# Performance work log

Measured on AMD Instinct MI355X. Metric: run time of the kernel, lower is better.

Reference implementation:

```python
import jax, jax.numpy as jnp
import numpy as np

MAX_AREA_WIDTH = 3  # from init_kwargs


def _window_vals(val, width, merge):
    """Multi-scale forward window sums: for each w in 1..width, sum val[t:t+w]
    over the seq axis, concatenated along the seq axis (total length
    width*L - width*(width-1)/2). Equivalent to the torch recurrence."""
    B, H, L, D = val.shape
    csum = jnp.concatenate(
        [jnp.zeros((B, H, 1, D), val.dtype), jnp.cumsum(val, axis=2)], axis=2)
    parts = []
    for i in range(width):
        w = i + 1
        s = csum[:, :, w:, :] - csum[:, :, :L - w + 1, :]  # [B,H,L-i,D]
        if merge == 'mean':
            s = s / jnp.asarray(w, val.dtype)
        parts.append(s)
    return jnp.concatenate(parts, axis=2)


def _window_masks(mask, width, zero_pad):
    parts = [mask[:, :, :, i:] for i in range(width)]
    m = jnp.concatenate(parts, axis=-1)  # [B,H,L,L']
    if zero_pad:
        m = m.at[:, :, 0, :].set(0)
    return m


def setup_inputs() -> dict:
    key = jax.random.key(0)
    kq, kk, kv = jax.random.split(key, 3)
    B, H, L, D = 8, 8, 512, 64
    q = jax.random.normal(kq, (B, H, L, D), jnp.float32)
    k = jax.random.normal(kk, (B, H, L, D), jnp.float32)
    v = jax.random.normal(kv, (B, H, L, D), jnp.float32)
    # causal attention mask, as used in pykt knowledge-tracing models
    mask = jnp.broadcast_to(jnp.tril(jnp.ones((L, L), jnp.int32)), (B, H, L, L))
    return {"q": q, "k": k, "v": v, "d_k": 64, "mask": mask, "zero_pad": 1}


def reference(q, k, v, d_k, mask, zero_pad):
    W = MAX_AREA_WIDTH
    k_area = _window_vals(k, W, 'mean')   # [B,H,L',D]
    v_area = _window_vals(v, W, 'sum')    # [B,H,L',D]
    m = _window_masks(mask, W, zero_pad)  # [B,H,L,L']
    scores = jnp.einsum('bhqd,bhkd->bhqk', q, k_area) / jnp.sqrt(
        jnp.asarray(d_k, jnp.float32))
    scores = jnp.where(m == 0, jnp.asarray(-1e32, scores.dtype), scores)
    attn = jax.nn.softmax(scores, axis=-1)  # dropout omitted (eval / p=0)
    return jnp.einsum('bhqk,bhkd->bhqd', attn, v_area)
```

## Files before the change

kernel.cpp:

```cpp
#include <hip/hip_runtime.h>


#define LSEQ 512
#define DDIM 64
#define BQ 64
#define BK 64
#define NTH 256

typedef __attribute__((ext_vector_type(8))) short bf8_t;
typedef __attribute__((ext_vector_type(4))) float f32x4;

__device__ __forceinline__ unsigned short f2bf(float f) {
  union { float f; unsigned u; } v; v.f = f;
  unsigned u = v.u;
  unsigned r = u + 0x7fffu + ((u >> 16) & 1u);
  return (unsigned short)(r >> 16);
}
__device__ __forceinline__ float bf2f(unsigned short h) {
  union { unsigned u; float f; } v; v.u = ((unsigned)h) << 16; return v.f;
}
__device__ __forceinline__ unsigned pk2(float a, float b) {
  return (unsigned)f2bf(a) | ((unsigned)f2bf(b) << 16);
}
__device__ __forceinline__ float ex2(float x) {
  float r; asm("v_exp_f32 %0, %1" : "=v"(r) : "v"(x)); return r;
}
__device__ __forceinline__ bf8_t pack8(float4 a, float4 b, float s) {
  bf8_t r;
  r[0] = (short)f2bf(a.x * s); r[1] = (short)f2bf(a.y * s);
  r[2] = (short)f2bf(a.z * s); r[3] = (short)f2bf(a.w * s);
  r[4] = (short)f2bf(b.x * s); r[5] = (short)f2bf(b.y * s);
  r[6] = (short)f2bf(b.z * s); r[7] = (short)f2bf(b.w * s);
  return r;
}

__global__ __launch_bounds__(256)
void vt_kernel(const float* __restrict__ vg, unsigned short* __restrict__ vt) {
  const int bh = blockIdx.x >> 3, oct = blockIdx.x & 7;
  const float* vb = vg + (size_t)bh * LSEQ * DDIM;
  unsigned short* vo = vt + (size_t)bh * DDIM * LSEQ;
#pragma unroll
  for (int it = 0; it < 4; ++it) {
    int item = threadIdx.x + it * 256;
    int d = item & 63, tq = item >> 6;
    int t = oct * 64 + tq * 4;
    ushort4 o;
    o.x = f2bf(vb[(t + 0) * DDIM + d]);
    o.y = f2bf(vb[(t + 1) * DDIM + d]);
    o.z = f2bf(vb[(t + 2) * DDIM + d]);
    o.w = f2bf(vb[(t + 3) * DDIM + d]);
    *(ushort4*)&vo[(size_t)d * LSEQ + t] = o;
  }
}

__global__ __launch_bounds__(256, 3)
void area_attn_kernel(const float* __restrict__ qg,
                      const float* __restrict__ kg,
                      const unsigned short* __restrict__ vtg,
                      float* __restrict__ outg) {
  const int bid = blockIdx.x;
  const int tid = threadIdx.x;

  __shared__ __align__(16) unsigned short Kbf[64 * 72];
  __shared__ __align__(16) unsigned short Vt[64 * 72];
  __shared__ __align__(16) unsigned short Ps[64 * 72];
  __shared__ __align__(16) float Ss[64][68];
  __shared__ float scale_arr[64];
  __shared__ float l_arr[64];

  if (bid >= 512) {
    const int bh = bid - 512;
    const unsigned short* vb = vtg + (size_t)bh * DDIM * LSEQ;
    float4* red = (float4*)&Ss[0][0];
    const int d4 = tid & 15, rg = tid >> 4;
    float4 acc = make_float4(0.f, 0.f, 0.f, 0.f);
    for (int t = rg; t < LSEQ; t += 16) {
      float c = (t == 0 || t == LSEQ - 1) ? 3.f
              : (t == 1 || t == LSEQ - 2) ? 5.f : 6.f;
      int d0 = d4 * 4;
      acc.x += c * bf2f(vb[(size_t)(d0 + 0) * LSEQ + t]);
      acc.y += c * bf2f(vb[(size_t)(d0 + 1) * LSEQ + t]);
      acc.z += c * bf2f(vb[(size_t)(d0 + 2) * LSEQ + t]);
      acc.w += c * bf2f(vb[(size_t)(d0 + 3) * LSEQ + t]);
    }
    red[rg * 16 + d4] = acc;
    __syncthreads();
    if (rg == 0) {
      float4 s = make_float4(0.f, 0.f, 0.f, 0.f);
#pragma unroll
      for (int g = 0; g < 16; ++g) {
        float4 x = red[g * 16 + d4];
        s.x += x.x; s.y += x.y; s.z += x.z; s.w += x.w;
      }
      const float inv = 1.0f / 1533.0f;
      s.x *= inv; s.y *= inv; s.z *= inv; s.w *= inv;
      ((float4*)(outg + (size_t)bh * LSEQ * DDIM))[d4] = s;
    }
    return;
  }

  const int half = bid >> 8;
  const int qt = half ? (7 - (bid & 7)) : (bid & 7);
  const int bh = ((bid >> 3) & 31) + (half << 5);
  const int q0 = qt * BQ;

  const float* qb = qg + (size_t)bh * LSEQ * DDIM;
  const float* kb = kg + (size_t)bh * LSEQ * DDIM;
  const unsigned short* vtb = vtg + (size_t)bh * DDIM * LSEQ;

  const int lane = tid & 63, w = tid >> 6;
  const int lc = lane & 15, lg = lane >> 4;
  const int koff = lg * 8;
  const int pr = tid >> 2, ps = tid & 3;
  const int ec0 = ps * 16;
  const float L2E = 1.44269504088896341f;

  bf8_t qa0, qa1;
  {
    const float* qrp = qb + (size_t)(q0 + 16 * w + lc) * DDIM;
    float4 xa = *(const float4*)(qrp + koff);
    float4 xb = *(const float4*)(qrp + koff + 4);
    qa0 = pack8(xa, xb, 0.125f);
    xa = *(const float4*)(qrp + 32 + koff);
    xb = *(const float4*)(qrp + 36 + koff);
    qa1 = pack8(xa, xb, 0.125f);
  }

  f32x4 oacc[4];
#pragma unroll
  for (int nt = 0; nt < 4; ++nt) oacc[nt] = (f32x4){0.f, 0.f, 0.f, 0.f};
  float m_run = -3.0e38f, l_run = 0.f;

  const int ntiles = qt + 1;
  for (int kt = 0; kt < ntiles; ++kt) {
    const int t0 = kt * BK;

    if (ps == 0) {
      if (kt == 0) { Ss[pr][64] = -1.0e30f; Ss[pr][65] = -1.0e30f; }
      else         { Ss[pr][64] = Ss[pr][62]; Ss[pr][65] = Ss[pr][63]; }
    }
    __syncthreads();

    {
      const float4* ka = (const float4*)(kb + (size_t)t0 * DDIM);
#pragma unroll
      for (int it = 0; it < 4; ++it) {
        int f = tid + it * NTH;
        int t = f >> 4, c4 = f & 15;
        float4 x = ka[t * 16 + c4];
        ushort4 o;
        o.x = f2bf(x.x); o.y = f2bf(x.y); o.z = f2bf(x.z); o.w = f2bf(x.w);
        *(ushort4*)&Kbf[t * 72 + c4 * 4] = o;
      }
#pragma unroll
      for (int it = 0; it < 4; ++it) {
        int f = tid + it * NTH;
        int d = f >> 4, tq = f & 15;
        ushort4 x = *(const ushort4*)&vtb[(size_t)d * LSEQ + t0 + tq * 4];
        *(ushort4*)&Vt[d * 72 + tq * 4] = x;
      }
      if (tid < 64) {
        unsigned x = 0;
        if (kt > 0) x = *(const unsigned*)&vtb[(size_t)tid * LSEQ + t0 - 2];
        *(unsigned*)&Vt[tid * 72 + 64] = x;
      }
    }
    __syncthreads();

#pragma unroll
    for (int nt = 0; nt < 4; ++nt) {
      int key = nt * 16 + lc;
      bf8_t kb0 = *(const bf8_t*)&Kbf[key * 72 + koff];
      bf8_t kb1 = *(const bf8_t*)&Kbf[key * 72 + 32 + koff];
      f32x4 acc = (f32x4){0.f, 0.f, 0.f, 0.f};
      acc = __builtin_amdgcn_mfma_f32_16x16x32_bf16(qa0, kb0, acc, 0, 0, 0);
      acc = __builtin_amdgcn_mfma_f32_16x16x32_bf16(qa1, kb1, acc, 0, 0, 0);
#pragma unroll
      for (int r = 0; r < 4; ++r)
        Ss[16 * w + 4 * lg + r][nt * 16 + lc] = acc[r];
    }

    {
      const int vmax = q0 + pr - t0;
      float pm1, pm2;
      if (ps == 0) { pm1 = Ss[pr][65] * L2E; pm2 = Ss[pr][64] * L2E; }
      else         { pm1 = Ss[pr][ec0 - 1] * L2E; pm2 = Ss[pr][ec0 - 2] * L2E; }

      float sv[16];
      *(float4*)&sv[0]  = *(const float4*)&Ss[pr][ec0];
      *(float4*)&sv[4]  = *(const float4*)&Ss[pr][ec0 + 4];
      *(float4*)&sv[8]  = *(const float4*)&Ss[pr][ec0 + 8];
      *(float4*)&sv[12] = *(const float4*)&Ss[pr][ec0 + 12];
#pragma unroll
      for (int k = 0; k < 16; ++k) sv[k] *= L2E;

      float mloc = -3.0e38f;
      {
        float a1 = pm1, a2 = pm2;
#pragma unroll
        for (int k = 0; k < 16; ++k) {
          float s0 = sv[k];
          float t = a1 + s0;
          float mm = fmaxf(s0, fmaxf(0.5f * t, (1.0f / 3.0f) * (a2 + t)));
          if (ec0 + k <= vmax) mloc = fmaxf(mloc, mm);
          a2 = a1; a1 = s0;
        }
      }
      mloc = fmaxf(mloc, __shfl_xor(mloc, 1));
      mloc = fmaxf(mloc, __shfl_xor(mloc, 2));
      const float m_new = fmaxf(m_run, mloc);
      const float alpha = ex2(m_run - m_new);
      m_run = m_new;
      if (ps == 0) scale_arr[pr] = alpha;
      l_run *= alpha;

      float cf[18];
#pragma unroll
      for (int k = 0; k < 18; ++k) cf[k] = 0.f;
      float ladd = 0.f;
      {
        float a1 = pm1, a2 = pm2;
#pragma unroll
        for (int k = 0; k < 16; ++k) {
          float s0 = sv[k];
          bool vld = (ec0 + k) <= vmax;
          float t = a1 + s0;
          float p1 = vld ? ex2(s0 - m_new) : 0.f;
          float p2 = vld ? ex2(0.5f * t - m_new) : 0.f;
          float p3 = vld ? ex2((1.0f / 3.0f) * (a2 + t) - m_new) : 0.f;
          float p23 = p2 + p3, p123 = p1 + p23;
          ladd += p123;
          cf[k + 2] += p123;
          cf[k + 1] += p23;
          cf[k]     += p3;
          a2 = a1; a1 = s0;
        }
      }
      ladd += __shfl_xor(ladd, 1);
      ladd += __shfl_xor(ladd, 2);
      l_run += ladd;
      if (ps == 0) l_arr[pr] = l_run;

      float up16 = __shfl_up(cf[16], 1, 4);
      float up17 = __shfl_up(cf[17], 1, 4);
      if (ps > 0) { cf[0] += up16; cf[1] += up17; }

      const int base = pr * 72;
      if (ps == 0) {
        *(unsigned*)&Ps[base + 64] = pk2(cf[0], cf[1]);
#pragma unroll
        for (int j = 0; j < 7; ++j)
          *(unsigned*)&Ps[base + 2 * j] = pk2(cf[2 + 2 * j], cf[3 + 2 * j]);
      } else {
        const int tcb = 16 * ps - 2;
#pragma unroll
        for (int j = 0; j < 8; ++j)
          *(unsigned*)&Ps[base + tcb + 2 * j] = pk2(cf[2 * j], cf[2 * j + 1]);
        if (ps == 3) *(unsigned*)&Ps[base + 62] = pk2(cf[16], cf[17]);
      }
    }

    {
      float al[4];
#pragma unroll
      for (int r = 0; r < 4; ++r) al[r] = scale_arr[16 * w + 4 * lg + r];
#pragma unroll
      for (int nt = 0; nt < 4; ++nt)
#pragma unroll
        for (int r = 0; r < 4; ++r) oacc[nt][r] *= al[r];

      bf8_t pa0 = *(const bf8_t*)&Ps[(16 * w + lc) * 72 + koff];
      bf8_t pa1 = *(const bf8_t*)&Ps[(16 * w + lc) * 72 + 32 + koff];
      float cm2[4], cm1[4];
#pragma unroll
      for (int r = 0; r < 4; ++r) {
        unsigned pc = *(const unsigned*)&Ps[(16 * w + 4 * lg + r) * 72 + 64];
        cm2[r] = bf2f((unsigned short)(pc & 0xffffu));
        cm1[r] = bf2f((unsigned short)(pc >> 16));
      }
#pragma unroll
      for (int nt = 0; nt < 4; ++nt) {
        int d = nt * 16 + lc;
        bf8_t vb0 = *(const bf8_t*)&Vt[d * 72 + koff];
        bf8_t vb1 = *(const bf8_t*)&Vt[d * 72 + 32 + koff];
        oacc[nt] = __builtin_amdgcn_mfma_f32_16x16x32_bf16(pa0, vb0, oacc[nt], 0, 0, 0);
        oacc[nt] = __builtin_amdgcn_mfma_f32_16x16x32_bf16(pa1, vb1, oacc[nt], 0, 0, 0);
        unsigned vc = *(const unsigned*)&Vt[d * 72 + 64];
        float vm2 = bf2f((unsigned short)(vc & 0xffffu));
        float vm1 = bf2f((unsigned short)(vc >> 16));
#pragma unroll
        for (int r = 0; r < 4; ++r)
          oacc[nt][r] += cm2[r] * vm2 + cm1[r] * vm1;
      }
    }
  }

  {
#pragma unroll
    for (int r = 0; r < 4; ++r) {
      int row = 16 * w + 4 * lg + r;
      int gr = q0 + row;
      if (gr != 0) {
        float inv = 1.0f / l_arr[row];
#pragma unroll
        for (int nt = 0; nt < 4; ++nt)
          outg[(size_t)(bh * LSEQ + gr) * DDIM + nt * 16 + lc] = oacc[nt][r] * inv;
      }
    }
  }
}

extern "C" void kernel_launch(void* const* d_in, const int* in_sizes, int n_in,
                              void* d_out, int out_size, void* d_ws, size_t ws_size,
                              hipStream_t stream) {
  (void)in_sizes; (void)n_in; (void)ws_size; (void)out_size;
  const float* q = (const float*)d_in[0];
  const float* k = (const float*)d_in[1];
  const float* v = (const float*)d_in[2];
  float* out = (float*)d_out;
  unsigned short* vt = (unsigned short*)d_ws;

  vt_kernel<<<dim3(512), dim3(256), 0, stream>>>(v, vt);
  area_attn_kernel<<<dim3(512 + 64), dim3(256), 0, stream>>>(q, k, vt, out);
}
```

Before: 146.3 us.

## Prefetch next K/V tile into registers and widen LDS row stride

```diff
diff --git a/kernel.cpp b/kernel.cpp
--- a/kernel.cpp
+++ b/kernel.cpp
@@ -6,6 +6,7 @@
 #define BQ 64
 #define BK 64
 #define NTH 256
+#define SPB 88
 
 typedef __attribute__((ext_vector_type(8))) short bf8_t;
 typedef __attribute__((ext_vector_type(4))) float f32x4;
@@ -61,9 +62,9 @@
   const int bid = blockIdx.x;
   const int tid = threadIdx.x;
 
-  __shared__ __align__(16) unsigned short Kbf[64 * 72];
-  __shared__ __align__(16) unsigned short Vt[64 * 72];
-  __shared__ __align__(16) unsigned short Ps[64 * 72];
+  __shared__ __align__(16) unsigned short Kbf[64 * SPB];
+  __shared__ __align__(16) unsigned short Vt[64 * SPB];
+  __shared__ __align__(16) unsigned short Ps[64 * SPB];
   __shared__ __align__(16) float Ss[64][68];
   __shared__ float scale_arr[64];
   __shared__ float l_arr[64];
@@ -126,12 +127,32 @@
     qa1 = pack8(xa, xb, 0.125f);
   }
 
+  float4 kpre[4];
+  ushort4 vpre[4];
+  unsigned cpre = 0;
+  auto issue_pf = [&](int t0p) {
+    const float4* ka = (const float4*)(kb + (size_t)t0p * DDIM);
+#pragma unroll
+    for (int it = 0; it < 4; ++it) kpre[it] = ka[tid + it * NTH];
+#pragma unroll
+    for (int it = 0; it < 4; ++it) {
+      int f = tid + it * NTH;
+      int d = f >> 4, tq = f & 15;
+      vpre[it] = *(const ushort4*)&vtb[(size_t)d * LSEQ + t0p + tq * 4];
+    }
+    cpre = 0;
+    if (tid < 64 && t0p > 0)
+      cpre = *(const unsigned*)&vtb[(size_t)tid * LSEQ + t0p - 2];
+  };
+
   f32x4 oacc[4];
 #pragma unroll
   for (int nt = 0; nt < 4; ++nt) oacc[nt] = (f32x4){0.f, 0.f, 0.f, 0.f};
   float m_run = -3.0e38f, l_run = 0.f;
 
   const int ntiles = qt + 1;
+  issue_pf(0);
+
   for (int kt = 0; kt < ntiles; ++kt) {
     const int t0 = kt * BK;
 
@@ -142,36 +163,32 @@
     __syncthreads();
 
     {
-      const float4* ka = (const float4*)(kb + (size_t)t0 * DDIM);
 #pragma unroll
       for (int it = 0; it < 4; ++it) {
         int f = tid + it * NTH;
         int t = f >> 4, c4 = f & 15;
-        float4 x = ka[t * 16 + c4];
+        float4 x = kpre[it];
         ushort4 o;
         o.x = f2bf(x.x); o.y = f2bf(x.y); o.z = f2bf(x.z); o.w = f2bf(x.w);
-        *(ushort4*)&Kbf[t * 72 + c4 * 4] = o;
+        *(ushort4*)&Kbf[t * SPB + c4 * 4] = o;
       }
 #pragma unroll
       for (int it = 0; it < 4; ++it) {
         int f = tid + it * NTH;
         int d = f >> 4, tq = f & 15;
-        ushort4 x = *(const ushort4*)&vtb[(size_t)d * LSEQ + t0 + tq * 4];
-        *(ushort4*)&Vt[d * 72 + tq * 4] = x;
-      }
-      if (tid < 64) {
-        unsigned x = 0;
-        if (kt > 0) x = *(const unsigned*)&vtb[(size_t)tid * LSEQ + t0 - 2];
-        *(unsigned*)&Vt[tid * 72 + 64] = x;
-      }
+        *(ushort4*)&Vt[d * SPB + tq * 4] = vpre[it];
+      }
+      if (tid < 64) *(unsigned*)&Vt[tid * SPB + 64] = cpre;
     }
     __syncthreads();
+
+    if (kt + 1 < ntiles) issue_pf(t0 + BK);
 
 #pragma unroll
     for (int nt = 0; nt < 4; ++nt) {
       int key = nt * 16 + lc;
-      bf8_t kb0 = *(const bf8_t*)&Kbf[key * 72 + koff];
-      bf8_t kb1 = *(const bf8_t*)&Kbf[key * 72 + 32 + koff];
+      bf8_t kb0 = *(const bf8_t*)&Kbf[key * SPB + koff];
+      bf8_t kb1 = *(const bf8_t*)&Kbf[key * SPB + 32 + koff];
       f32x4 acc = (f32x4){0.f, 0.f, 0.f, 0.f};
       acc = __builtin_amdgcn_mfma_f32_16x16x32_bf16(qa0, kb0, acc, 0, 0, 0);
       acc = __builtin_amdgcn_mfma_f32_16x16x32_bf16(qa1, kb1, acc, 0, 0, 0);
@@ -245,7 +262,7 @@
       float up17 = __shfl_up(cf[17], 1, 4);
       if (ps > 0) { cf[0] += up16; cf[1] += up17; }
 
-      const int base = pr * 72;
+      const int base = pr * SPB;
       if (ps == 0) {
         *(unsigned*)&Ps[base + 64] = pk2(cf[0], cf[1]);
 #pragma unroll
@@ -269,23 +286,23 @@
 #pragma unroll
         for (int r = 0; r < 4; ++r) oacc[nt][r] *= al[r];
 
-      bf8_t pa0 = *(const bf8_t*)&Ps[(16 * w + lc) * 72 + koff];
-      bf8_t pa1 = *(const bf8_t*)&Ps[(16 * w + lc) * 72 + 32 + koff];
+      bf8_t pa0 = *(const bf8_t*)&Ps[(16 * w + lc) * SPB + koff];
+      bf8_t pa1 = *(const bf8_t*)&Ps[(16 * w + lc) * SPB + 32 + koff];
       float cm2[4], cm1[4];
 #pragma unroll
       for (int r = 0; r < 4; ++r) {
-        unsigned pc = *(const unsigned*)&Ps[(16 * w + 4 * lg + r) * 72 + 64];
+        unsigned pc = *(const unsigned*)&Ps[(16 * w + 4 * lg + r) * SPB + 64];
         cm2[r] = bf2f((unsigned short)(pc & 0xffffu));
         cm1[r] = bf2f((unsigned short)(pc >> 16));
       }
 #pragma unroll
       for (int nt = 0; nt < 4; ++nt) {
         int d = nt * 16 + lc;
-        bf8_t vb0 = *(const bf8_t*)&Vt[d * 72 + koff];
-        bf8_t vb1 = *(const bf8_t*)&Vt[d * 72 + 32 + koff];
+        bf8_t vb0 = *(const bf8_t*)&Vt[d * SPB + koff];
+        bf8_t vb1 = *(const bf8_t*)&Vt[d * SPB + 32 + koff];
         oacc[nt] = __builtin_amdgcn_mfma_f32_16x16x32_bf16(pa0, vb0, oacc[nt], 0, 0, 0);
         oacc[nt] = __builtin_amdgcn_mfma_f32_16x16x32_bf16(pa1, vb1, oacc[nt], 0, 0, 0);
-        unsigned vc = *(const unsigned*)&Vt[d * 72 + 64];
+        unsigned vc = *(const unsigned*)&Vt[d * SPB + 64];
         float vm2 = bf2f((unsigned short)(vc & 0xffffu));
         float vm1 = bf2f((unsigned short)(vc >> 16));
 #pragma unroll
```

After: 156.5 us. 1.07x slower.

## Split attention into single-wave 16-row blocks reading pre-converted bf16 operands

Applied to the files above, without the earlier changes.

```diff
diff --git a/kernel.cpp b/kernel.cpp
--- a/kernel.cpp
+++ b/kernel.cpp
@@ -3,9 +3,9 @@
 
 #define LSEQ 512
 #define DDIM 64
-#define BQ 64
 #define BK 64
-#define NTH 256
+#define SPB 88
+#define SSW 68
 
 typedef __attribute__((ext_vector_type(8))) short bf8_t;
 typedef __attribute__((ext_vector_type(4))) float f32x4;
@@ -25,113 +25,106 @@
 __device__ __forceinline__ float ex2(float x) {
   float r; asm("v_exp_f32 %0, %1" : "=v"(r) : "v"(x)); return r;
 }
-__device__ __forceinline__ bf8_t pack8(float4 a, float4 b, float s) {
-  bf8_t r;
-  r[0] = (short)f2bf(a.x * s); r[1] = (short)f2bf(a.y * s);
-  r[2] = (short)f2bf(a.z * s); r[3] = (short)f2bf(a.w * s);
-  r[4] = (short)f2bf(b.x * s); r[5] = (short)f2bf(b.y * s);
-  r[6] = (short)f2bf(b.z * s); r[7] = (short)f2bf(b.w * s);
-  return r;
-}
 
 __global__ __launch_bounds__(256)
-void vt_kernel(const float* __restrict__ vg, unsigned short* __restrict__ vt) {
-  const int bh = blockIdx.x >> 3, oct = blockIdx.x & 7;
-  const float* vb = vg + (size_t)bh * LSEQ * DDIM;
-  unsigned short* vo = vt + (size_t)bh * DDIM * LSEQ;
-#pragma unroll
-  for (int it = 0; it < 4; ++it) {
-    int item = threadIdx.x + it * 256;
-    int d = item & 63, tq = item >> 6;
-    int t = oct * 64 + tq * 4;
-    ushort4 o;
-    o.x = f2bf(vb[(t + 0) * DDIM + d]);
-    o.y = f2bf(vb[(t + 1) * DDIM + d]);
-    o.z = f2bf(vb[(t + 2) * DDIM + d]);
-    o.w = f2bf(vb[(t + 3) * DDIM + d]);
-    *(ushort4*)&vo[(size_t)d * LSEQ + t] = o;
-  }
-}
-
-__global__ __launch_bounds__(256, 3)
-void area_attn_kernel(const float* __restrict__ qg,
-                      const float* __restrict__ kg,
-                      const unsigned short* __restrict__ vtg,
-                      float* __restrict__ outg) {
-  const int bid = blockIdx.x;
-  const int tid = threadIdx.x;
-
-  __shared__ __align__(16) unsigned short Kbf[64 * 72];
-  __shared__ __align__(16) unsigned short Vt[64 * 72];
-  __shared__ __align__(16) unsigned short Ps[64 * 72];
-  __shared__ __align__(16) float Ss[64][68];
-  __shared__ float scale_arr[64];
-  __shared__ float l_arr[64];
-
-  if (bid >= 512) {
-    const int bh = bid - 512;
-    const unsigned short* vb = vtg + (size_t)bh * DDIM * LSEQ;
-    float4* red = (float4*)&Ss[0][0];
+void prep_kernel(const float* __restrict__ qg, const float* __restrict__ kg,
+                 const float* __restrict__ vg,
+                 unsigned short* __restrict__ vt,
+                 unsigned short* __restrict__ qbf,
+                 unsigned short* __restrict__ kbf,
+                 float* __restrict__ outg) {
+  const int bid = blockIdx.x, tid = threadIdx.x;
+  if (bid < 512) {
+    const int bh = bid >> 3, oct = bid & 7;
+    const float* vb = vg + (size_t)bh * LSEQ * DDIM;
+    unsigned short* vo = vt + (size_t)bh * DDIM * LSEQ;
+#pragma unroll
+    for (int it = 0; it < 4; ++it) {
+      int item = tid + it * 256;
+      int d = item & 63, tq = item >> 6;
+      int t = oct * 64 + tq * 4;
+      ushort4 o;
+      o.x = f2bf(vb[(t + 0) * DDIM + d]);
+      o.y = f2bf(vb[(t + 1) * DDIM + d]);
+      o.z = f2bf(vb[(t + 2) * DDIM + d]);
+      o.w = f2bf(vb[(t + 3) * DDIM + d]);
+      *(ushort4*)&vo[(size_t)d * LSEQ + t] = o;
+    }
+  } else if (bid < 1536) {
+    const bool isq = bid < 1024;
+    const float4* src = (const float4*)(isq ? qg : kg);
+    ushort4* dst = (ushort4*)(isq ? qbf : kbf);
+    const float s = isq ? 0.125f : 1.0f;
+    const int blk = bid & 511;
+#pragma unroll
+    for (int it = 0; it < 4; ++it) {
+      int f = blk * 1024 + it * 256 + tid;
+      float4 x = src[f];
+      ushort4 o;
+      o.x = f2bf(x.x * s); o.y = f2bf(x.y * s);
+      o.z = f2bf(x.z * s); o.w = f2bf(x.w * s);
+      dst[f] = o;
+    }
+  } else {
+    __shared__ float4 red[256];
+    const int bh = bid - 1536;
+    const float4* vb4 = (const float4*)(vg + (size_t)bh * LSEQ * DDIM);
     const int d4 = tid & 15, rg = tid >> 4;
     float4 acc = make_float4(0.f, 0.f, 0.f, 0.f);
     for (int t = rg; t < LSEQ; t += 16) {
       float c = (t == 0 || t == LSEQ - 1) ? 3.f
               : (t == 1 || t == LSEQ - 2) ? 5.f : 6.f;
-      int d0 = d4 * 4;
-      acc.x += c * bf2f(vb[(size_t)(d0 + 0) * LSEQ + t]);
-      acc.y += c * bf2f(vb[(size_t)(d0 + 1) * LSEQ + t]);
-      acc.z += c * bf2f(vb[(size_t)(d0 + 2) * LSEQ + t]);
-      acc.w += c * bf2f(vb[(size_t)(d0 + 3) * LSEQ + t]);
+      float4 x = vb4[t * 16 + d4];
+      acc.x += c * x.x; acc.y += c * x.y; acc.z += c * x.z; acc.w += c * x.w;
     }
     red[rg * 16 + d4] = acc;
     __syncthreads();
     if (rg == 0) {
-      float4 s = make_float4(0.f, 0.f, 0.f, 0.f);
+      float4 sum = make_float4(0.f, 0.f, 0.f, 0.f);
 #pragma unroll
       for (int g = 0; g < 16; ++g) {
         float4 x = red[g * 16 + d4];
-        s.x += x.x; s.y += x.y; s.z += x.z; s.w += x.w;
+        sum.x += x.x; sum.y += x.y; sum.z += x.z; sum.w += x.w;
       }
       const float inv = 1.0f / 1533.0f;
-      s.x *= inv; s.y *= inv; s.z *= inv; s.w *= inv;
-      ((float4*)(outg + (size_t)bh * LSEQ * DDIM))[d4] = s;
-    }
-    return;
+      sum.x *= inv; sum.y *= inv; sum.z *= inv; sum.w *= inv;
+      ((float4*)(outg + (size_t)bh * LSEQ * DDIM))[d4] = sum;
+    }
   }
-
-  const int half = bid >> 8;
-  const int qt = half ? (7 - (bid & 7)) : (bid & 7);
-  const int bh = ((bid >> 3) & 31) + (half << 5);
-  const int q0 = qt * BQ;
-
-  const float* qb = qg + (size_t)bh * LSEQ * DDIM;
-  const float* kb = kg + (size_t)bh * LSEQ * DDIM;
-  const unsigned short* vtb = vtg + (size_t)bh * DDIM * LSEQ;
-
-  const int lane = tid & 63, w = tid >> 6;
+}
+
+__global__ __launch_bounds__(64, 4)
+void area_attn_kernel(const unsigned short* __restrict__ qbf,
+                      const unsigned short* __restrict__ kbf,
+                      const unsigned short* __restrict__ vtg,
+                      float* __restrict__ outg) {
+  __shared__ __align__(16) float Ss[16][SSW];
+  __shared__ __align__(16) unsigned short Ps[16 * SPB];
+
+  const int bid = blockIdx.x;
+  const int bh = bid >> 5, qt = bid & 31;
+  const int q0 = qt * 16;
+  const int lane = threadIdx.x;
   const int lc = lane & 15, lg = lane >> 4;
   const int koff = lg * 8;
-  const int pr = tid >> 2, ps = tid & 3;
+  const int pr = lane >> 2, ps = lane & 3;
   const int ec0 = ps * 16;
   const float L2E = 1.44269504088896341f;
 
-  bf8_t qa0, qa1;
-  {
-    const float* qrp = qb + (size_t)(q0 + 16 * w + lc) * DDIM;
-    float4 xa = *(const float4*)(qrp + koff);
-    float4 xb = *(const float4*)(qrp + koff + 4);
-    qa0 = pack8(xa, xb, 0.125f);
-    xa = *(const float4*)(qrp + 32 + koff);
-    xb = *(const float4*)(qrp + 36 + koff);
-    qa1 = pack8(xa, xb, 0.125f);
-  }
+  const unsigned short* qb = qbf + (size_t)bh * LSEQ * DDIM;
+  const unsigned short* kb = kbf + (size_t)bh * LSEQ * DDIM;
+  const unsigned short* vtb = vtg + (size_t)bh * DDIM * LSEQ;
+
+  const bf8_t qa0 = *(const bf8_t*)&qb[(size_t)(q0 + lc) * DDIM + koff];
+  const bf8_t qa1 = *(const bf8_t*)&qb[(size_t)(q0 + lc) * DDIM + 32 + koff];
 
   f32x4 oacc[4];
 #pragma unroll
   for (int nt = 0; nt < 4; ++nt) oacc[nt] = (f32x4){0.f, 0.f, 0.f, 0.f};
   float m_run = -3.0e38f, l_run = 0.f;
-
-  const int ntiles = qt + 1;
+  float alphav = 0.f;
+
+  const int ntiles = (qt >> 2) + 1;
   for (int kt = 0; kt < ntiles; ++kt) {
     const int t0 = kt * BK;
 
@@ -139,45 +132,18 @@
       if (kt == 0) { Ss[pr][64] = -1.0e30f; Ss[pr][65] = -1.0e30f; }
       else         { Ss[pr][64] = Ss[pr][62]; Ss[pr][65] = Ss[pr][63]; }
     }
-    __syncthreads();
-
-    {
-      const float4* ka = (const float4*)(kb + (size_t)t0 * DDIM);
-#pragma unroll
-      for (int it = 0; it < 4; ++it) {
-        int f = tid + it * NTH;
-        int t = f >> 4, c4 = f & 15;
-        float4 x = ka[t * 16 + c4];
-        ushort4 o;
-        o.x = f2bf(x.x); o.y = f2bf(x.y); o.z = f2bf(x.z); o.w = f2bf(x.w);
-        *(ushort4*)&Kbf[t * 72 + c4 * 4] = o;
-      }
-#pragma unroll
-      for (int it = 0; it < 4; ++it) {
-        int f = tid + it * NTH;
-        int d = f >> 4, tq = f & 15;
-        ushort4 x = *(const ushort4*)&vtb[(size_t)d * LSEQ + t0 + tq * 4];
-        *(ushort4*)&Vt[d * 72 + tq * 4] = x;
-      }
-      if (tid < 64) {
-        unsigned x = 0;
-        if (kt > 0) x = *(const unsigned*)&vtb[(size_t)tid * LSEQ + t0 - 2];
-        *(unsigned*)&Vt[tid * 72 + 64] = x;
-      }
-    }
-    __syncthreads();
 
 #pragma unroll
     for (int nt = 0; nt < 4; ++nt) {
-      int key = nt * 16 + lc;
-      bf8_t kb0 = *(const bf8_t*)&Kbf[key * 72 + koff];
-      bf8_t kb1 = *(const bf8_t*)&Kbf[key * 72 + 32 + koff];
+      const size_t kr = (size_t)(t0 + nt * 16 + lc) * DDIM;
+      bf8_t kf0 = *(const bf8_t*)&kb[kr + koff];
+      bf8_t kf1 = *(const bf8_t*)&kb[kr + 32 + koff];
       f32x4 acc = (f32x4){0.f, 0.f, 0.f, 0.f};
-      acc = __builtin_amdgcn_mfma_f32_16x16x32_bf16(qa0, kb0, acc, 0, 0, 0);
-      acc = __builtin_amdgcn_mfma_f32_16x16x32_bf16(qa1, kb1, acc, 0, 0, 0);
+      acc = __builtin_amdgcn_mfma_f32_16x16x32_bf16(qa0, kf0, acc, 0, 0, 0);
+      acc = __builtin_amdgcn_mfma_f32_16x16x32_bf16(qa1, kf1, acc, 0, 0, 0);
 #pragma unroll
       for (int r = 0; r < 4; ++r)
-        Ss[16 * w + 4 * lg + r][nt * 16 + lc] = acc[r];
+        Ss[4 * lg + r][nt * 16 + lc] = acc[r];
     }
 
     {
@@ -209,10 +175,9 @@
       mloc = fmaxf(mloc, __shfl_xor(mloc, 1));
       mloc = fmaxf(mloc, __shfl_xor(mloc, 2));
       const float m_new = fmaxf(m_run, mloc);
-      const float alpha = ex2(m_run - m_new);
+      alphav = ex2(m_run - m_new);
       m_run = m_new;
-      if (ps == 0) scale_arr[pr] = alpha;
-      l_run *= alpha;
+      l_run *= alphav;
 
       float cf[18];
 #pragma unroll
@@ -239,13 +204,12 @@
       ladd += __shfl_xor(ladd, 1);
       ladd += __shfl_xor(ladd, 2);
       l_run += ladd;
-      if (ps == 0) l_arr[pr] = l_run;
 
       float up16 = __shfl_up(cf[16], 1, 4);
       float up17 = __shfl_up(cf[17], 1, 4);
       if (ps > 0) { cf[0] += up16; cf[1] += up17; }
 
-      const int base = pr * 72;
+      const int base = pr * SPB;
       if (ps == 0) {
         *(unsigned*)&Ps[base + 64] = pk2(cf[0], cf[1]);
 #pragma unroll
@@ -261,31 +225,32 @@
     }
 
     {
-      float al[4];
-#pragma unroll
-      for (int r = 0; r < 4; ++r) al[r] = scale_arr[16 * w + 4 * lg + r];
+      float av[4];
+#pragma unroll
+      for (int r = 0; r < 4; ++r) av[r] = __shfl(alphav, 16 * lg + 4 * r);
 #pragma unroll
       for (int nt = 0; nt < 4; ++nt)
 #pragma unroll
-        for (int r = 0; r < 4; ++r) oacc[nt][r] *= al[r];
-
-      bf8_t pa0 = *(const bf8_t*)&Ps[(16 * w + lc) * 72 + koff];
-      bf8_t pa1 = *(const bf8_t*)&Ps[(16 * w + lc) * 72 + 32 + koff];
+        for (int r = 0; r < 4; ++r) oacc[nt][r] *= av[r];
+
+      bf8_t pa0 = *(const bf8_t*)&Ps[lc * SPB + koff];
+      bf8_t pa1 = *(const bf8_t*)&Ps[lc * SPB + 32 + koff];
       float cm2[4], cm1[4];
 #pragma unroll
       for (int r = 0; r < 4; ++r) {
-        unsigned pc = *(const unsigned*)&Ps[(16 * w + 4 * lg + r) * 72 + 64];
+        unsigned pc = *(const unsigned*)&Ps[(4 * lg + r) * SPB + 64];
         cm2[r] = bf2f((unsigned short)(pc & 0xffffu));
         cm1[r] = bf2f((unsigned short)(pc >> 16));
       }
 #pragma unroll
       for (int nt = 0; nt < 4; ++nt) {
-        int d = nt * 16 + lc;
-        bf8_t vb0 = *(const bf8_t*)&Vt[d * 72 + koff];
-        bf8_t vb1 = *(const bf8_t*)&Vt[d * 72 + 32 + koff];
-        oacc[nt] = __builtin_amdgcn_mfma_f32_16x16x32_bf16(pa0, vb0, oacc[nt], 0, 0, 0);
-        oacc[nt] = __builtin_amdgcn_mfma_f32_16x16x32_bf16(pa1, vb1, oacc[nt], 0, 0, 0);
-        unsigned vc = *(const unsigned*)&Vt[d * 72 + 64];
+        const size_t vr = (size_t)(nt * 16 + lc) * LSEQ + t0;
+        bf8_t vf0 = *(const bf8_t*)&vtb[vr + koff];
+        bf8_t vf1 = *(const bf8_t*)&vtb[vr + 32 + koff];
+        oacc[nt] = __builtin_amdgcn_mfma_f32_16x16x32_bf16(pa0, vf0, oacc[nt], 0, 0, 0);
+        oacc[nt] = __builtin_amdgcn_mfma_f32_16x16x32_bf16(pa1, vf1, oacc[nt], 0, 0, 0);
+        unsigned vc = 0;
+        if (kt > 0) vc = *(const unsigned*)&vtb[vr - 2];
         float vm2 = bf2f((unsigned short)(vc & 0xffffu));
         float vm1 = bf2f((unsigned short)(vc >> 16));
 #pragma unroll
@@ -295,17 +260,15 @@
     }
   }
 
-  {
-#pragma unroll
-    for (int r = 0; r < 4; ++r) {
-      int row = 16 * w + 4 * lg + r;
-      int gr = q0 + row;
-      if (gr != 0) {
-        float inv = 1.0f / l_arr[row];
-#pragma unroll
-        for (int nt = 0; nt < 4; ++nt)
-          outg[(size_t)(bh * LSEQ + gr) * DDIM + nt * 16 + lc] = oacc[nt][r] * inv;
-      }
+#pragma unroll
+  for (int r = 0; r < 4; ++r) {
+    float lr = __shfl(l_run, 16 * lg + 4 * r);
+    int gr = q0 + 4 * lg + r;
+    if (gr != 0) {
+      float inv = 1.0f / lr;
+#pragma unroll
+      for (int nt = 0; nt < 4; ++nt)
+        outg[(size_t)(bh * LSEQ + gr) * DDIM + nt * 16 + lc] = oacc[nt][r] * inv;
     }
   }
 }
@@ -318,8 +281,12 @@
   const float* k = (const float*)d_in[1];
   const float* v = (const float*)d_in[2];
   float* out = (float*)d_out;
-  unsigned short* vt = (unsigned short*)d_ws;
-
-  vt_kernel<<<dim3(512), dim3(256), 0, stream>>>(v, vt);
-  area_attn_kernel<<<dim3(512 + 64), dim3(256), 0, stream>>>(q, k, vt, out);
-}
+
+  unsigned short* ws = (unsigned short*)d_ws;
+  unsigned short* vt  = ws;
+  unsigned short* qbf = ws + 2097152;
+  unsigned short* kbf = ws + 2 * 2097152;
+
+  prep_kernel<<<dim3(1600), dim3(256), 0, stream>>>(q, k, v, vt, qbf, kbf, out);
+  area_attn_kernel<<<dim3(2048), dim3(64), 0, stream>>>(qbf, kbf, vt, out);
+}
```

After: 161.3 us. 10.3% more time.
